# Performance work log

Hardware: AMD Instinct MI355X
Metric: run time of the kernel (lower is better)

Reference implementation:

```python
import jax, jax.numpy as jnp
import numpy as np

EPS = 1e-12  # torch F.normalize eps

def _l2_normalize(x):
    # torch.nn.functional.normalize(x, dim=1, p=2): x / max(||x||, eps)
    norm = jnp.sqrt(jnp.sum(x * x, axis=1, keepdims=True))
    return x / jnp.maximum(norm, EPS)

def setup_inputs() -> dict:
    key = jax.random.key(0)
    k1, k2 = jax.random.split(key)
    B, N, D = 128, 1_000_000, 128
    vectors = jax.random.normal(k1, (B, D), dtype=jnp.float32)
    db_vectors = jax.random.normal(k2, (N, D), dtype=jnp.float32)
    return {"vectors": vectors, "db_vectors": db_vectors, "k": 10}

def reference(vectors, db_vectors, k):
    # DB normalization happens once in __init__; queries normalized per call.
    db_n = _l2_normalize(db_vectors)          # [N, D]
    q_n = _l2_normalize(vectors)              # [B, D]
    similarities = q_n @ db_n.T               # [B, N] cosine similarities
    _, indices = jax.lax.top_k(similarities, k)
    return indices, similarities
```

## Files before the change

### kernel.cpp

```cpp
#include <hip/hip_runtime.h>

#define EPS 1e-12f
#define NEG_INF (-3.0e38f)

constexpr int B = 128;
constexpr int D = 128;
constexpr int K_TOP = 10;
constexpr int TILE_N = 128;

typedef _Float16 half8 __attribute__((ext_vector_type(8)));
typedef _Float16 half4v __attribute__((ext_vector_type(4)));
typedef float f32x4 __attribute__((ext_vector_type(4)));

__device__ inline unsigned fkey(float f) {
    unsigned u = __float_as_uint(f);
    return u ^ (((int)u >> 31) | 0x80000000u);
}
__device__ inline float kinv(unsigned k) {
    unsigned u = k ^ (((int)(~k) >> 31) | 0x80000000u);
    return __uint_as_float(u);
}

__global__ void qprep_kernel(const float* __restrict__ q, _Float16* __restrict__ qA) {
    int r = blockIdx.x, l = threadIdx.x;
    float2 v = *(const float2*)(q + r * D + 2 * l);
    float s = v.x * v.x + v.y * v.y;
#pragma unroll
    for (int off = 32; off > 0; off >>= 1) s += __shfl_xor(s, off);
    float iv = 1.0f / fmaxf(sqrtf(s), EPS);
    float qx = v.x * iv, qy = v.y * iv;
    _Float16 hx = (_Float16)qx, hy = (_Float16)qy;
    _Float16 lx = (_Float16)(qx - (float)hx), ly = (_Float16)(qy - (float)hy);
    int k = 2 * l;
    int o = ((r >> 4) * 4 + (k >> 5)) * 512 + ((k >> 3) & 3) * 128 + ((r & 15) << 3) + (k & 7);
    _Float16* qhi = qA;
    _Float16* qlo = qA + 16384;
    qhi[o] = hx; qhi[o + 1] = hy;
    qlo[o] = lx; qlo[o + 1] = ly;
}

__global__ void initkeys_kernel(unsigned* __restrict__ keys, int total) {
    int i = blockIdx.x * 256 + threadIdx.x;
    int stride = gridDim.x * 256;
    for (; i < total; i += stride) keys[i] = 0u;
}

__global__ __launch_bounds__(256, 2)
void simgemm_kernel(const _Float16* __restrict__ qA, const float* __restrict__ db,
                    float* __restrict__ sim, unsigned* __restrict__ keys,
                    int N, int ngroups, int gshift) {
    __shared__ _Float16 Bhi[TILE_N * 128];
    __shared__ _Float16 Blo[TILE_N * 128];
    __shared__ float inv_db[TILE_N];

    const int t = threadIdx.x;
    const int l = t & 63, w = t >> 6;
    const int n0 = blockIdx.x * TILE_N;

    const half8* qhi = (const half8*)qA;
    const half8* qlo = qhi + 2048;
    half8 ahi[2][4], alo[2][4];
#pragma unroll
    for (int mi = 0; mi < 2; ++mi)
#pragma unroll
        for (int ks = 0; ks < 4; ++ks) {
            int fi = (w * 2 + mi) * 4 + ks;
            ahi[mi][ks] = qhi[fi * 64 + l];
            alo[mi][ks] = qlo[fi * 64 + l];
        }

#pragma unroll
    for (int it = 0; it < 16; ++it) {
        int f = t + 256 * it;
        int row = f >> 5, c4 = f & 31;
        int gr = n0 + row;
        float4 v = make_float4(0.f, 0.f, 0.f, 0.f);
        if (gr < N) v = *(const float4*)(db + (size_t)gr * D + c4 * 4);
        float s = v.x * v.x + v.y * v.y + v.z * v.z + v.w * v.w;
        s += __shfl_xor(s, 1);  s += __shfl_xor(s, 2);  s += __shfl_xor(s, 4);
        s += __shfl_xor(s, 8);  s += __shfl_xor(s, 16);
        if ((t & 31) == 0) inv_db[row] = 1.0f / fmaxf(sqrtf(s), EPS);
        _Float16 h0 = (_Float16)v.x, h1 = (_Float16)v.y, h2 = (_Float16)v.z, h3 = (_Float16)v.w;
        half4v hh = {h0, h1, h2, h3};
        half4v ll = {(_Float16)(v.x - (float)h0), (_Float16)(v.y - (float)h1),
                     (_Float16)(v.z - (float)h2), (_Float16)(v.w - (float)h3)};
        int addr = (row * 256 + c4 * 8) ^ ((row & 7) << 4);
        *(half4v*)((char*)Bhi + addr) = hh;
        *(half4v*)((char*)Blo + addr) = ll;
    }
    __syncthreads();

    const int cmod = l & 15, rgrp = l >> 4;
    f32x4 acc[2][8];
#pragma unroll
    for (int mi = 0; mi < 2; ++mi)
#pragma unroll
        for (int nj = 0; nj < 8; ++nj) acc[mi][nj] = (f32x4){0.f, 0.f, 0.f, 0.f};

#pragma unroll
    for (int ks = 0; ks < 4; ++ks) {
#pragma unroll
        for (int nj = 0; nj < 8; ++nj) {
            int nl = nj * 16 + cmod;
            int addr = (nl * 256 + ks * 64 + rgrp * 16) ^ ((nl & 7) << 4);
            half8 bh = *(const half8*)((const char*)Bhi + addr);
            half8 bl = *(const half8*)((const char*)Blo + addr);
#pragma unroll
            for (int mi = 0; mi < 2; ++mi) {
                acc[mi][nj] = __builtin_amdgcn_mfma_f32_16x16x32_f16(alo[mi][ks], bh, acc[mi][nj], 0, 0, 0);
                acc[mi][nj] = __builtin_amdgcn_mfma_f32_16x16x32_f16(ahi[mi][ks], bl, acc[mi][nj], 0, 0, 0);
                acc[mi][nj] = __builtin_amdgcn_mfma_f32_16x16x32_f16(ahi[mi][ks], bh, acc[mi][nj], 0, 0, 0);
            }
        }
    }

    float inv[8];
#pragma unroll
    for (int nj = 0; nj < 8; ++nj) inv[nj] = inv_db[nj * 16 + cmod];

    const int grp = blockIdx.x >> gshift;
#pragma unroll
    for (int mi = 0; mi < 2; ++mi) {
#pragma unroll
        for (int r = 0; r < 4; ++r) {
            const int row = w * 32 + mi * 16 + rgrp * 4 + r;
            float rowmax = NEG_INF;
            float* srow = sim + (size_t)row * N;
#pragma unroll
            for (int nj = 0; nj < 8; ++nj) {
                int gn = n0 + nj * 16 + cmod;
                float val = acc[mi][nj][r] * inv[nj];
                if (gn < N) { srow[gn] = val; rowmax = fmaxf(rowmax, val); }
            }
#pragma unroll
            for (int off = 8; off > 0; off >>= 1)
                rowmax = fmaxf(rowmax, __shfl_xor(rowmax, off));
            if (cmod == 0)
                atomicMax(&keys[(size_t)row * ngroups + grp], fkey(rowmax));
        }
    }
}

__global__ __launch_bounds__(256)
void topk_kernel(const float* __restrict__ sim, const unsigned* __restrict__ keys,
                 float* __restrict__ out_idx, int N, int ngroups, int gshift) {
    const int q = blockIdx.x, t = threadIdx.x;
    const unsigned* krow = keys + (size_t)q * ngroups;
    const float* srow = sim + (size_t)q * N;

    unsigned kv[10];
#pragma unroll
    for (int j = 0; j < 10; ++j) kv[j] = 0;
    for (int gi = t; gi < ngroups; gi += 256) {
        unsigned x = krow[gi];
        if (x > kv[9]) {
#pragma unroll
            for (int j = 9; j >= 1; --j) {
                if (kv[j - 1] < x)      kv[j] = kv[j - 1];
                else if (kv[j] < x)     kv[j] = x;
            }
            if (kv[0] < x)              kv[0] = x;
        }
    }
    __shared__ unsigned skv[2560];
#pragma unroll
    for (int j = 0; j < 10; ++j) skv[t * 10 + j] = kv[j];
    __syncthreads();
    __shared__ unsigned srv[256];
    __shared__ int srs[256];
    unsigned Tkey = 0;
    for (int r = 0; r < K_TOP; ++r) {
        unsigned bv = 0; int bslot = t * 10;
#pragma unroll
        for (int j = 0; j < 10; ++j) {
            int s2 = t * 10 + j;
            if (skv[s2] > bv) { bv = skv[s2]; bslot = s2; }
        }
        srv[t] = bv; srs[t] = bslot;
        __syncthreads();
        for (int s2 = 128; s2 > 0; s2 >>= 1) {
            if (t < s2 && srv[t + s2] > srv[t]) { srv[t] = srv[t + s2]; srs[t] = srs[t + s2]; }
            __syncthreads();
        }
        Tkey = srv[0];
        if (t == 0) skv[srs[0]] = 0;
        __syncthreads();
    }
    float Tf = (Tkey == 0) ? NEG_INF : kinv(Tkey);

    float cv[10]; int ci[10];
#pragma unroll
    for (int j = 0; j < 10; ++j) { cv[j] = NEG_INF; ci[j] = 0x7fffffff; }
    const int gcols = TILE_N << gshift;
    for (int gi = t; gi < ngroups; gi += 256) {
        if (krow[gi] >= Tkey) {
            int c0 = gi * gcols;
            int c1 = min(c0 + gcols, N);
            for (int c = c0; c < c1; c += 4) {
                float4 x4 = *(const float4*)(srow + c);
#pragma unroll
                for (int cc = 0; cc < 4; ++cc) {
                    float xv = (cc == 0) ? x4.x : (cc == 1) ? x4.y : (cc == 2) ? x4.z : x4.w;
                    if (xv >= Tf && xv > cv[9]) {
                        int n = c + cc;
#pragma unroll
                        for (int j = 9; j >= 1; --j) {
                            if (cv[j - 1] < xv)      { cv[j] = cv[j - 1]; ci[j] = ci[j - 1]; }
                            else if (cv[j] < xv)     { cv[j] = xv;        ci[j] = n;         }
                        }
                        if (cv[0] < xv)              { cv[0] = xv;        ci[0] = n;         }
                    }
                }
            }
        }
    }

    __shared__ float lv[2560];
    __shared__ int   li[2560];
#pragma unroll
    for (int j = 0; j < 10; ++j) { lv[t * 10 + j] = cv[j]; li[t * 10 + j] = ci[j]; }
    __syncthreads();
    __shared__ float rv[256];
    __shared__ int   ri[256];
    __shared__ int   rs2[256];
    for (int r = 0; r < K_TOP; ++r) {
        float bv = NEG_INF; int bi = 0x7fffffff; int bslot = t * 10;
#pragma unroll
        for (int j = 0; j < 10; ++j) {
            int s2 = t * 10 + j;
            float vv = lv[s2]; int ii = li[s2];
            if (vv > bv || (vv == bv && ii < bi)) { bv = vv; bi = ii; bslot = s2; }
        }
        rv[t] = bv; ri[t] = bi; rs2[t] = bslot;
        __syncthreads();
        for (int s2 = 128; s2 > 0; s2 >>= 1) {
            if (t < s2) {
                if (rv[t + s2] > rv[t] || (rv[t + s2] == rv[t] && ri[t + s2] < ri[t])) {
                    rv[t] = rv[t + s2]; ri[t] = ri[t + s2]; rs2[t] = rs2[t + s2];
                }
            }
            __syncthreads();
        }
        if (t == 0) {
            out_idx[q * K_TOP + r] = (float)ri[0];
            lv[rs2[0]] = NEG_INF;
        }
        __syncthreads();
    }
}

extern "C" void kernel_launch(void* const* d_in, const int* in_sizes, int n_in,
                              void* d_out, int out_size, void* d_ws, size_t ws_size,
                              hipStream_t stream) {
    const float* vec = (const float*)d_in[0];
    const float* db  = (const float*)d_in[1];
    const int N  = in_sizes[1] / D;
    const int NT = (N + TILE_N - 1) / TILE_N;

    float* out_idx = (float*)d_out;
    float* sim     = (float*)d_out + B * K_TOP;

    _Float16* qA   = (_Float16*)d_ws;
    unsigned* keys = (unsigned*)((char*)d_ws + 65536);

    int gshift = 0, ngroups = NT;
    while (gshift < 12) {
        ngroups = (NT + (1 << gshift) - 1) >> gshift;
        if (65536 + (size_t)B * ngroups * 4 <= ws_size) break;
        ++gshift;
    }
    ngroups = (NT + (1 << gshift) - 1) >> gshift;

    qprep_kernel<<<B, 64, 0, stream>>>(vec, qA);
    initkeys_kernel<<<1024, 256, 0, stream>>>(keys, B * ngroups);
    simgemm_kernel<<<NT, 256, 0, stream>>>(qA, db, sim, keys, N, ngroups, gshift);
    topk_kernel<<<B, 256, 0, stream>>>(sim, keys, out_idx, N, ngroups, gshift);
}
```

Measured before the change: 1.095 ms.

## Make similarity GEMM persistent with register prefetch of next DB tile

Turns the similarity kernel into a persistent kernel of up to 512 blocks, each walking tiles with a grid stride. While a block converts the current tile into LDS and runs the MFMA and store phases, the next tile's fp32 rows are already being loaded into registers, so global load latency overlaps compute and the large sim writes. This adds 64 VGPRs per thread for the prefetch buffer, which may hurt occupancy under launch_bounds(256,2). It also relies on explicit barriers around LDS reuse.

```diff
diff --git a/kernel.cpp b/kernel.cpp
--- a/kernel.cpp
+++ b/kernel.cpp
@@ -48,14 +48,19 @@
 __global__ __launch_bounds__(256, 2)
 void simgemm_kernel(const _Float16* __restrict__ qA, const float* __restrict__ db,
                     float* __restrict__ sim, unsigned* __restrict__ keys,
-                    int N, int ngroups, int gshift) {
+                    int N, int NT, int ngroups, int gshift) {
     __shared__ _Float16 Bhi[TILE_N * 128];
     __shared__ _Float16 Blo[TILE_N * 128];
     __shared__ float inv_db[TILE_N];
 
     const int t = threadIdx.x;
     const int l = t & 63, w = t >> 6;
-    const int n0 = blockIdx.x * TILE_N;
+    const int c4 = t & 31;
+    const int r0 = t >> 5;
+    const int cmod = l & 15, rgrp = l >> 4;
+
+    int tile = blockIdx.x;
+    if (tile >= NT) return;
 
     const half8* qhi = (const half8*)qA;
     const half8* qlo = qhi + 2048;
@@ -69,75 +74,105 @@
             alo[mi][ks] = qlo[fi * 64 + l];
         }
 
+    float4 v[16];
 #pragma unroll
     for (int it = 0; it < 16; ++it) {
-        int f = t + 256 * it;
-        int row = f >> 5, c4 = f & 31;
-        int gr = n0 + row;
-        float4 v = make_float4(0.f, 0.f, 0.f, 0.f);
-        if (gr < N) v = *(const float4*)(db + (size_t)gr * D + c4 * 4);
-        float s = v.x * v.x + v.y * v.y + v.z * v.z + v.w * v.w;
-        s += __shfl_xor(s, 1);  s += __shfl_xor(s, 2);  s += __shfl_xor(s, 4);
-        s += __shfl_xor(s, 8);  s += __shfl_xor(s, 16);
-        if ((t & 31) == 0) inv_db[row] = 1.0f / fmaxf(sqrtf(s), EPS);
-        _Float16 h0 = (_Float16)v.x, h1 = (_Float16)v.y, h2 = (_Float16)v.z, h3 = (_Float16)v.w;
-        half4v hh = {h0, h1, h2, h3};
-        half4v ll = {(_Float16)(v.x - (float)h0), (_Float16)(v.y - (float)h1),
-                     (_Float16)(v.z - (float)h2), (_Float16)(v.w - (float)h3)};
-        int addr = (row * 256 + c4 * 8) ^ ((row & 7) << 4);
-        *(half4v*)((char*)Bhi + addr) = hh;
-        *(half4v*)((char*)Blo + addr) = ll;
-    }
-    __syncthreads();
-
-    const int cmod = l & 15, rgrp = l >> 4;
-    f32x4 acc[2][8];
-#pragma unroll
-    for (int mi = 0; mi < 2; ++mi)
-#pragma unroll
-        for (int nj = 0; nj < 8; ++nj) acc[mi][nj] = (f32x4){0.f, 0.f, 0.f, 0.f};
-
-#pragma unroll
-    for (int ks = 0; ks < 4; ++ks) {
-#pragma unroll
-        for (int nj = 0; nj < 8; ++nj) {
-            int nl = nj * 16 + cmod;
-            int addr = (nl * 256 + ks * 64 + rgrp * 16) ^ ((nl & 7) << 4);
-            half8 bh = *(const half8*)((const char*)Bhi + addr);
-            half8 bl = *(const half8*)((const char*)Blo + addr);
-#pragma unroll
-            for (int mi = 0; mi < 2; ++mi) {
-                acc[mi][nj] = __builtin_amdgcn_mfma_f32_16x16x32_f16(alo[mi][ks], bh, acc[mi][nj], 0, 0, 0);
-                acc[mi][nj] = __builtin_amdgcn_mfma_f32_16x16x32_f16(ahi[mi][ks], bl, acc[mi][nj], 0, 0, 0);
-                acc[mi][nj] = __builtin_amdgcn_mfma_f32_16x16x32_f16(ahi[mi][ks], bh, acc[mi][nj], 0, 0, 0);
-            }
-        }
-    }
-
-    float inv[8];
-#pragma unroll
-    for (int nj = 0; nj < 8; ++nj) inv[nj] = inv_db[nj * 16 + cmod];
-
-    const int grp = blockIdx.x >> gshift;
-#pragma unroll
-    for (int mi = 0; mi < 2; ++mi) {
-#pragma unroll
-        for (int r = 0; r < 4; ++r) {
-            const int row = w * 32 + mi * 16 + rgrp * 4 + r;
-            float rowmax = NEG_INF;
-            float* srow = sim + (size_t)row * N;
+        int gr = tile * TILE_N + r0 + 8 * it;
+        float4 x = make_float4(0.f, 0.f, 0.f, 0.f);
+        if (gr < N) x = *(const float4*)(db + (size_t)gr * D + c4 * 4);
+        v[it] = x;
+    }
+
+    while (true) {
+        const int n0 = tile * TILE_N;
+
+        asm volatile("s_waitcnt lgkmcnt(0)" ::: "memory");
+        __builtin_amdgcn_sched_barrier(0);
+        __builtin_amdgcn_s_barrier();
+
+#pragma unroll
+        for (int it = 0; it < 16; ++it) {
+            int row = r0 + 8 * it;
+            float4 x = v[it];
+            float s = x.x * x.x + x.y * x.y + x.z * x.z + x.w * x.w;
+            s += __shfl_xor(s, 1);  s += __shfl_xor(s, 2);  s += __shfl_xor(s, 4);
+            s += __shfl_xor(s, 8);  s += __shfl_xor(s, 16);
+            if (c4 == 0) inv_db[row] = 1.0f / fmaxf(sqrtf(s), EPS);
+            _Float16 h0 = (_Float16)x.x, h1 = (_Float16)x.y, h2 = (_Float16)x.z, h3 = (_Float16)x.w;
+            half4v hh = {h0, h1, h2, h3};
+            half4v ll = {(_Float16)(x.x - (float)h0), (_Float16)(x.y - (float)h1),
+                         (_Float16)(x.z - (float)h2), (_Float16)(x.w - (float)h3)};
+            int addr = (row * 256 + c4 * 8) ^ ((row & 7) << 4);
+            *(half4v*)((char*)Bhi + addr) = hh;
+            *(half4v*)((char*)Blo + addr) = ll;
+        }
+
+        const int next = tile + (int)gridDim.x;
+        if (next < NT) {
+#pragma unroll
+            for (int it = 0; it < 16; ++it) {
+                int gr = next * TILE_N + r0 + 8 * it;
+                float4 x = make_float4(0.f, 0.f, 0.f, 0.f);
+                if (gr < N) x = *(const float4*)(db + (size_t)gr * D + c4 * 4);
+                v[it] = x;
+            }
+        }
+
+        asm volatile("s_waitcnt lgkmcnt(0)" ::: "memory");
+        __builtin_amdgcn_sched_barrier(0);
+        __builtin_amdgcn_s_barrier();
+
+        f32x4 acc[2][8];
+#pragma unroll
+        for (int mi = 0; mi < 2; ++mi)
+#pragma unroll
+            for (int nj = 0; nj < 8; ++nj) acc[mi][nj] = (f32x4){0.f, 0.f, 0.f, 0.f};
+
+#pragma unroll
+        for (int ks = 0; ks < 4; ++ks) {
 #pragma unroll
             for (int nj = 0; nj < 8; ++nj) {
-                int gn = n0 + nj * 16 + cmod;
-                float val = acc[mi][nj][r] * inv[nj];
-                if (gn < N) { srow[gn] = val; rowmax = fmaxf(rowmax, val); }
-            }
-#pragma unroll
-            for (int off = 8; off > 0; off >>= 1)
-                rowmax = fmaxf(rowmax, __shfl_xor(rowmax, off));
-            if (cmod == 0)
-                atomicMax(&keys[(size_t)row * ngroups + grp], fkey(rowmax));
-        }
+                int nl = nj * 16 + cmod;
+                int addr = (nl * 256 + ks * 64 + rgrp * 16) ^ ((nl & 7) << 4);
+                half8 bh = *(const half8*)((const char*)Bhi + addr);
+                half8 bl = *(const half8*)((const char*)Blo + addr);
+#pragma unroll
+                for (int mi = 0; mi < 2; ++mi) {
+                    acc[mi][nj] = __builtin_amdgcn_mfma_f32_16x16x32_f16(alo[mi][ks], bh, acc[mi][nj], 0, 0, 0);
+                    acc[mi][nj] = __builtin_amdgcn_mfma_f32_16x16x32_f16(ahi[mi][ks], bl, acc[mi][nj], 0, 0, 0);
+                    acc[mi][nj] = __builtin_amdgcn_mfma_f32_16x16x32_f16(ahi[mi][ks], bh, acc[mi][nj], 0, 0, 0);
+                }
+            }
+        }
+
+        float inv[8];
+#pragma unroll
+        for (int nj = 0; nj < 8; ++nj) inv[nj] = inv_db[nj * 16 + cmod];
+
+        const int grp = tile >> gshift;
+#pragma unroll
+        for (int mi = 0; mi < 2; ++mi) {
+#pragma unroll
+            for (int r = 0; r < 4; ++r) {
+                const int row = w * 32 + mi * 16 + rgrp * 4 + r;
+                float rowmax = NEG_INF;
+                float* srow = sim + (size_t)row * N;
+#pragma unroll
+                for (int nj = 0; nj < 8; ++nj) {
+                    int gn = n0 + nj * 16 + cmod;
+                    float val = acc[mi][nj][r] * inv[nj];
+                    if (gn < N) { srow[gn] = val; rowmax = fmaxf(rowmax, val); }
+                }
+#pragma unroll
+                for (int off = 8; off > 0; off >>= 1)
+                    rowmax = fmaxf(rowmax, __shfl_xor(rowmax, off));
+                if (cmod == 0)
+                    atomicMax(&keys[(size_t)row * ngroups + grp], fkey(rowmax));
+            }
+        }
+
+        if (next >= NT) break;
+        tile = next;
     }
 }
 
@@ -271,8 +306,12 @@
     }
     ngroups = (NT + (1 << gshift) - 1) >> gshift;
 
+    int nblocks = 512;
+    if (nblocks > NT) nblocks = NT;
+    if (nblocks < 1)  nblocks = 1;
+
     qprep_kernel<<<B, 64, 0, stream>>>(vec, qA);
     initkeys_kernel<<<1024, 256, 0, stream>>>(keys, B * ngroups);
-    simgemm_kernel<<<NT, 256, 0, stream>>>(qA, db, sim, keys, N, ngroups, gshift);
+    simgemm_kernel<<<nblocks, 256, 0, stream>>>(qA, db, sim, keys, N, NT, ngroups, gshift);
     topk_kernel<<<B, 256, 0, stream>>>(sim, keys, out_idx, N, ngroups, gshift);
 }
```

Result: slower. 1.175 ms (+7.3%).
